# Performance work log

Hardware: AMD Instinct MI355X
Metric: run time of the kernel (lower is better)

## Reference

```python
import jax, jax.numpy as jnp
import numpy as np

SEQ_LEN = 512
EMBED_DIM = 768
MAX_SPAN_LEN = 16
WIDTH_EMB_DIM = 50
NUM_SPAN_LABELS = 9
N_SPANS = 32768


def setup_inputs() -> dict:
    key = jax.random.key(0)
    ks = jax.random.split(key, 6)
    sequence_output = jax.random.normal(ks[0], (1, SEQ_LEN, EMBED_DIM), dtype=jnp.float32)
    # start in [0, SEQ_LEN - MAX_SPAN_LEN) so end = start + width stays a valid index
    start_indices = jax.random.randint(ks[1], (N_SPANS,), 0, SEQ_LEN - MAX_SPAN_LEN)
    span_widths = jax.random.randint(ks[2], (N_SPANS,), 1, MAX_SPAN_LEN + 1)  # width >= 1 (mean over non-empty slice)
    end_indices = start_indices + span_widths
    width_table = jax.random.normal(ks[3], (MAX_SPAN_LEN + 1, WIDTH_EMB_DIM), dtype=jnp.float32) * 0.02
    W = jax.random.normal(ks[4], (NUM_SPAN_LABELS, 3 * EMBED_DIM + WIDTH_EMB_DIM), dtype=jnp.float32) * 0.02
    b = jnp.zeros((NUM_SPAN_LABELS,), dtype=jnp.float32)
    return {
        "sequence_output": sequence_output,
        "start_indices": start_indices,
        "end_indices": end_indices,
        "span_widths": span_widths,
        "width_table": width_table,
        "W": W,
        "b": b,
    }


def reference(sequence_output, start_indices, end_indices, span_widths, width_table, W, b):
    # sequence_output: [1, S, D]; batch is asserted to be 1 in the original module.
    seq = sequence_output[0]                       # [S, D]
    h_start = seq[start_indices]                   # [N, D] gather of start tokens
    h_end = seq[end_indices]                       # [N, D] gather of end tokens
    # Ragged mean over seq[s:e] (exclusive end), vectorized via exclusive prefix sums:
    # mean = (cumsum[e] - cumsum[s]) / (e - s)
    cs = jnp.concatenate([jnp.zeros((1, seq.shape[-1]), seq.dtype), jnp.cumsum(seq, axis=0)], axis=0)  # [S+1, D]
    widths_f = span_widths[:, None].astype(seq.dtype)
    h_span_avg = (cs[end_indices] - cs[start_indices]) / widths_f   # [N, D]
    width_emb = width_table[span_widths]            # [N, 50]
    span_rep = jnp.concatenate([h_start, h_end, h_span_avg, width_emb], axis=-1)  # [N, 3D+50]
    logits = span_rep @ W.T + b                     # [N, num_labels]
    return logits
```

## Files before the change

kernel.cpp:

```cpp
#include <hip/hip_runtime.h>

#define SEQ_LEN 512
#define EMBED_DIM 768
#define WIDTH_EMB 50
#define NUM_LABELS 9
#define N_SPANS 32768
#define WROW (3 * EMBED_DIM + WIDTH_EMB)

#define P1_OFF 0
#define P2_OFF (SEQ_LEN * NUM_LABELS)
#define P3_OFF (2 * SEQ_LEN * NUM_LABELS)
#define WP_OFF (3 * SEQ_LEN * NUM_LABELS)

__global__ __launch_bounds__(64) void proj_kernel(
    const float* __restrict__ seq,
    const float* __restrict__ wtab,
    const float* __restrict__ W,
    const float* __restrict__ b,
    float* __restrict__ ws)
{
    const int blk  = blockIdx.x;
    const int lane = threadIdx.x;

    if (blk < SEQ_LEN) {
        const float2* srow = (const float2*)(seq + blk * EMBED_DIM);
        float2 s2[6];
#pragma unroll
        for (int k = 0; k < 6; ++k) s2[k] = srow[lane + 64 * k];

#pragma unroll
        for (int seg = 0; seg < 3; ++seg) {
#pragma unroll
            for (int l = 0; l < NUM_LABELS; ++l) {
                const float2* wrow =
                    (const float2*)(W + l * WROW + seg * EMBED_DIM);
                float p = 0.f;
#pragma unroll
                for (int k = 0; k < 6; ++k) {
                    float2 wv = wrow[lane + 64 * k];
                    p += s2[k].x * wv.x + s2[k].y * wv.y;
                }
#pragma unroll
                for (int off = 32; off > 0; off >>= 1)
                    p += __shfl_xor(p, off, 64);
                if (lane == 0)
                    ws[seg * (SEQ_LEN * NUM_LABELS) + blk * NUM_LABELS + l] = p;
            }
        }
    } else {
        for (int idx = lane; idx < 17 * NUM_LABELS; idx += 64) {
            int w = idx / NUM_LABELS;
            int l = idx - w * NUM_LABELS;
            const float* wrow = W + l * WROW + 3 * EMBED_DIM;
            const float* trow = wtab + w * WIDTH_EMB;
            float p = b[l];
            for (int j = 0; j < WIDTH_EMB; ++j) p += trow[j] * wrow[j];
            ws[WP_OFF + idx] = p;
        }
    }
}

#define SPB 64
__global__ __launch_bounds__(576) void span_kernel(
    const int* __restrict__ start_idx,
    const int* __restrict__ end_idx,
    const int* __restrict__ widths,
    const float* __restrict__ ws,
    float* __restrict__ out)
{
    __shared__ float sP3[SEQ_LEN * NUM_LABELS];
    __shared__ float sWP[17 * NUM_LABELS];

    const int t = threadIdx.x;
    for (int i = t; i < SEQ_LEN * NUM_LABELS; i += 576)
        sP3[i] = ws[P3_OFF + i];
    if (t < 17 * NUM_LABELS)
        sWP[t] = ws[WP_OFF + t];
    __syncthreads();

    const int n = blockIdx.x * SPB + t / NUM_LABELS;
    const int l = t - (t / NUM_LABELS) * NUM_LABELS;

    const int s = start_idx[n];
    const int e = end_idx[n];
    const int w = widths[n];

    float acc = ws[P1_OFF + s * NUM_LABELS + l]
              + ws[P2_OFF + e * NUM_LABELS + l]
              + sWP[w * NUM_LABELS + l];
    float sum = 0.f;
    for (int k = s; k < e; ++k) sum += sP3[k * NUM_LABELS + l];
    out[blockIdx.x * (SPB * NUM_LABELS) + t] = acc + sum / (float)w;
}

extern "C" void kernel_launch(void* const* d_in, const int* in_sizes, int n_in,
                              void* d_out, int out_size, void* d_ws, size_t ws_size,
                              hipStream_t stream) {
    const float* seq  = (const float*)d_in[0];
    const int*   s    = (const int*)d_in[1];
    const int*   e    = (const int*)d_in[2];
    const int*   w    = (const int*)d_in[3];
    const float* wtab = (const float*)d_in[4];
    const float* W    = (const float*)d_in[5];
    const float* b    = (const float*)d_in[6];
    float* out = (float*)d_out;
    float* ws  = (float*)d_ws;

    proj_kernel<<<SEQ_LEN + 1, 64, 0, stream>>>(seq, wtab, W, b, ws);

    span_kernel<<<N_SPANS / SPB, 576, 0, stream>>>(s, e, w, ws, out);
}
```

Baseline: 83.04 us.

## Replace per-span ragged loop with prefix-sum scan and widen projection blocks

```diff
diff --git a/kernel.cpp b/kernel.cpp
--- a/kernel.cpp
+++ b/kernel.cpp
@@ -10,54 +10,88 @@
 #define P1_OFF 0
 #define P2_OFF (SEQ_LEN * NUM_LABELS)
 #define P3_OFF (2 * SEQ_LEN * NUM_LABELS)
-#define WP_OFF (3 * SEQ_LEN * NUM_LABELS)
+#define C3_OFF (3 * SEQ_LEN * NUM_LABELS)
+#define WP_OFF (C3_OFF + (SEQ_LEN + 1) * NUM_LABELS)
 
-__global__ __launch_bounds__(64) void proj_kernel(
+__global__ __launch_bounds__(576) void proj_kernel(
     const float* __restrict__ seq,
     const float* __restrict__ wtab,
     const float* __restrict__ W,
     const float* __restrict__ b,
     float* __restrict__ ws)
 {
-    const int blk  = blockIdx.x;
-    const int lane = threadIdx.x;
+    const int blk = blockIdx.x;
+    const int t   = threadIdx.x;
 
     if (blk < SEQ_LEN) {
+        const int l    = t >> 6;
+        const int lane = t & 63;
+
         const float2* srow = (const float2*)(seq + blk * EMBED_DIM);
         float2 s2[6];
 #pragma unroll
         for (int k = 0; k < 6; ++k) s2[k] = srow[lane + 64 * k];
 
+        const float2* wbase = (const float2*)(W + l * WROW);
+        float p[3] = {0.f, 0.f, 0.f};
 #pragma unroll
         for (int seg = 0; seg < 3; ++seg) {
 #pragma unroll
-            for (int l = 0; l < NUM_LABELS; ++l) {
-                const float2* wrow =
-                    (const float2*)(W + l * WROW + seg * EMBED_DIM);
-                float p = 0.f;
-#pragma unroll
-                for (int k = 0; k < 6; ++k) {
-                    float2 wv = wrow[lane + 64 * k];
-                    p += s2[k].x * wv.x + s2[k].y * wv.y;
-                }
-#pragma unroll
-                for (int off = 32; off > 0; off >>= 1)
-                    p += __shfl_xor(p, off, 64);
-                if (lane == 0)
-                    ws[seg * (SEQ_LEN * NUM_LABELS) + blk * NUM_LABELS + l] = p;
+            for (int k = 0; k < 6; ++k) {
+                float2 wv = wbase[seg * 384 + lane + 64 * k];
+                p[seg] += s2[k].x * wv.x + s2[k].y * wv.y;
             }
         }
+#pragma unroll
+        for (int seg = 0; seg < 3; ++seg) {
+#pragma unroll
+            for (int off = 32; off > 0; off >>= 1)
+                p[seg] += __shfl_xor(p[seg], off, 64);
+        }
+        if (lane == 0) {
+            ws[P1_OFF + blk * NUM_LABELS + l] = p[0];
+            ws[P2_OFF + blk * NUM_LABELS + l] = p[1];
+            ws[P3_OFF + blk * NUM_LABELS + l] = p[2];
+        }
     } else {
-        for (int idx = lane; idx < 17 * NUM_LABELS; idx += 64) {
+        for (int idx = t; idx < 17 * NUM_LABELS; idx += 576) {
             int w = idx / NUM_LABELS;
             int l = idx - w * NUM_LABELS;
             const float* wrow = W + l * WROW + 3 * EMBED_DIM;
             const float* trow = wtab + w * WIDTH_EMB;
-            float p = b[l];
-            for (int j = 0; j < WIDTH_EMB; ++j) p += trow[j] * wrow[j];
-            ws[WP_OFF + idx] = p;
+            float pp = b[l];
+#pragma unroll
+            for (int j = 0; j < WIDTH_EMB; ++j) pp += trow[j] * wrow[j];
+            ws[WP_OFF + idx] = pp;
         }
     }
+}
+
+__global__ __launch_bounds__(576) void scan_kernel(float* __restrict__ ws)
+{
+    const int l    = threadIdx.x >> 6;
+    const int lane = threadIdx.x & 63;
+
+    float v[8];
+#pragma unroll
+    for (int j = 0; j < 8; ++j)
+        v[j] = ws[P3_OFF + (lane * 8 + j) * NUM_LABELS + l];
+#pragma unroll
+    for (int j = 1; j < 8; ++j) v[j] += v[j - 1];
+
+    const float lsum = v[7];
+    float sc = lsum;
+#pragma unroll
+    for (int off = 1; off < 64; off <<= 1) {
+        float u = __shfl_up(sc, off, 64);
+        if (lane >= off) sc += u;
+    }
+    const float excl = sc - lsum;
+
+#pragma unroll
+    for (int j = 0; j < 8; ++j)
+        ws[C3_OFF + (lane * 8 + j + 1) * NUM_LABELS + l] = excl + v[j];
+    if (lane == 0) ws[C3_OFF + l] = 0.f;
 }
 
 #define SPB 64
@@ -68,29 +102,23 @@
     const float* __restrict__ ws,
     float* __restrict__ out)
 {
-    __shared__ float sP3[SEQ_LEN * NUM_LABELS];
-    __shared__ float sWP[17 * NUM_LABELS];
-
-    const int t = threadIdx.x;
-    for (int i = t; i < SEQ_LEN * NUM_LABELS; i += 576)
-        sP3[i] = ws[P3_OFF + i];
-    if (t < 17 * NUM_LABELS)
-        sWP[t] = ws[WP_OFF + t];
-    __syncthreads();
-
-    const int n = blockIdx.x * SPB + t / NUM_LABELS;
-    const int l = t - (t / NUM_LABELS) * NUM_LABELS;
+    const int t  = threadIdx.x;
+    const int sp = t / NUM_LABELS;
+    const int l  = t - sp * NUM_LABELS;
+    const int n  = blockIdx.x * SPB + sp;
 
     const int s = start_idx[n];
     const int e = end_idx[n];
     const int w = widths[n];
 
-    float acc = ws[P1_OFF + s * NUM_LABELS + l]
-              + ws[P2_OFF + e * NUM_LABELS + l]
-              + sWP[w * NUM_LABELS + l];
-    float sum = 0.f;
-    for (int k = s; k < e; ++k) sum += sP3[k * NUM_LABELS + l];
-    out[blockIdx.x * (SPB * NUM_LABELS) + t] = acc + sum / (float)w;
+    const float c = (ws[C3_OFF + e * NUM_LABELS + l]
+                   - ws[C3_OFF + s * NUM_LABELS + l]) / (float)w;
+
+    out[blockIdx.x * (SPB * NUM_LABELS) + t] =
+          ws[P1_OFF + s * NUM_LABELS + l]
+        + ws[P2_OFF + e * NUM_LABELS + l]
+        + ws[WP_OFF + w * NUM_LABELS + l]
+        + c;
 }
 
 extern "C" void kernel_launch(void* const* d_in, const int* in_sizes, int n_in,
@@ -106,7 +134,7 @@
     float* out = (float*)d_out;
     float* ws  = (float*)d_ws;
 
-    proj_kernel<<<SEQ_LEN + 1, 64, 0, stream>>>(seq, wtab, W, b, ws);
-
+    proj_kernel<<<SEQ_LEN + 1, 576, 0, stream>>>(seq, wtab, W, b, ws);
+    scan_kernel<<<1, 576, 0, stream>>>(ws);
     span_kernel<<<N_SPANS / SPB, 576, 0, stream>>>(s, e, w, ws, out);
 }
```

Measured after the change: 78.03 us. -6.0%, faster.
